# Optimization experiments

Hardware: AMD Instinct MI355X
Metric: run time of the kernel (lower is better)

The kernel has to match this reference:

```python
import jax, jax.numpy as jnp
import numpy as np

B, C, L, H, K, NCONV = 16, 128, 1024, 8, 7, 4
DK = C // H
EPS = 1e-5
NEG = -1e30


def setup_inputs() -> dict:
    key = jax.random.key(0)
    ks = jax.random.split(key, 20)
    s = 0.05
    rn = lambda k, shape: jax.random.normal(k, shape, jnp.float32) * s
    return {
        "x": jax.random.normal(ks[0], (B, C, L), jnp.float32),
        "mask": jax.random.bernoulli(ks[1], 0.1, (B, L)),
        "dw_w": rn(ks[2], (NCONV, C, K)),
        "pw_w": rn(ks[3], (NCONV, C, C)),
        "pw_b": rn(ks[4], (NCONV, C)),
        "ng": jnp.ones((NCONV + 2, C), jnp.float32),
        "nb": jnp.zeros((NCONV + 2, C), jnp.float32),
        "wq": rn(ks[5], (C, C)), "bq": rn(ks[6], (C,)),
        "wk": rn(ks[7], (C, C)), "bk": rn(ks[8], (C,)),
        "wv": rn(ks[9], (C, C)), "bv": rn(ks[10], (C,)),
        "wo": rn(ks[11], (C, C)), "bo": rn(ks[12], (C,)),
        "w1": rn(ks[13], (C, C)), "b1": rn(ks[14], (C,)),
        "w2": rn(ks[15], (C, C)), "b2": rn(ks[16], (C,)),
    }


def _pos_encoding(c, length):
    i = jnp.arange(c, dtype=jnp.float32)
    even = (jnp.arange(c) % 2) == 0
    freq = jnp.where(even, jnp.power(10000.0, -i / c), -jnp.power(10000.0, (1.0 - i) / c))
    phase = jnp.where(even, 0.0, jnp.pi / 2)
    pos = jnp.arange(length, dtype=jnp.float32)
    return jnp.sin(pos[None, :] * freq[:, None] + phase[:, None])  # [C, L]


def _ln(x, g, b):
    # layer norm over channel dim of [B, C, L]
    mu = jnp.mean(x, axis=1, keepdims=True)
    var = jnp.mean(jnp.square(x - mu), axis=1, keepdims=True)
    xn = (x - mu) * jax.lax.rsqrt(var + EPS)
    return xn * g[None, :, None] + b[None, :, None]


def _dsconv(x, dw, pw, pb):
    # depthwise conv1d (groups=C, pad k//2, no bias) + pointwise conv1d (bias)
    y = jax.lax.conv_general_dilated(
        x, dw[:, None, :], window_strides=(1,), padding=[(K // 2, K // 2)],
        feature_group_count=C, dimension_numbers=("NCH", "OIH", "NCH"))
    return jnp.einsum("oc,bcl->bol", pw, y) + pb[None, :, None]


def _attention(x, mask, wq, bq, wk, bk, wv, bv, wo, bo):
    # x: [B, C, L] -> [B, L, C]
    xt = jnp.swapaxes(x, 1, 2)
    q = (xt @ wq.T + bq).reshape(B, L, H, DK)
    k = (xt @ wk.T + bk).reshape(B, L, H, DK)
    v = (xt @ wv.T + bv).reshape(B, L, H, DK)
    scale = 1.0 / np.sqrt(DK)
    scores = jnp.einsum("blhd,bmhd->bhlm", q, k) * scale  # [B, H, L, L]
    scores = jnp.where(mask[:, None, None, :], NEG, scores)
    attn = jax.nn.softmax(scores, axis=-1)
    out = jnp.einsum("bhlm,bmhd->blhd", attn, v).reshape(B, L, C)
    out = out @ wo.T + bo
    return jnp.swapaxes(out, 1, 2)  # [B, C, L]


def reference(x, mask, dw_w, pw_w, pw_b, ng, nb, wq, bq, wk, bk, wv, bv, wo, bo, w1, b1, w2, b2):
    # eval mode: all dropout / stochastic depth are identity
    out = x + _pos_encoding(C, L)[None]
    for i in range(NCONV):
        res = out
        out = _ln(out, ng[i], nb[i])
        out = _dsconv(out, dw_w[i], pw_w[i], pw_b[i])
        out = jax.nn.relu(out)
        out = out + res
    res = out
    out = _ln(out, ng[NCONV], nb[NCONV])
    out = _attention(out, mask, wq, bq, wk, bk, wv, bv, wo, bo)
    out = out + res
    res = out
    out = _ln(out, ng[NCONV + 1], nb[NCONV + 1])
    ot = jnp.swapaxes(out, 1, 2)
    ot = jax.nn.relu(ot @ w1.T + b1)
    ot = ot @ w2.T + b2
    out = jnp.swapaxes(ot, 1, 2) + res
    return out
```

## Files before the change

### kernel.cpp

```cpp
#include <hip/hip_runtime.h>
#include <math.h>


#define ACT_N   2097152
#define OFF_ACT0 0
#define OFF_ACT1 (ACT_N)
#define OFF_QB   (2*ACT_N)
#define OFF_KB   (3*ACT_N)
#define OFF_VT   (4*ACT_N)
#define OFF_ABF  (5*ACT_N)
#define OFF_MF   (6*ACT_N)
#define OFF_WB   (6*ACT_N + 16384)
#define OFF_DW8  (6*ACT_N + 16384 + 81920)

typedef __attribute__((ext_vector_type(8)))  short bf16x8;
typedef __attribute__((ext_vector_type(16))) float f32x16;
typedef __attribute__((ext_vector_type(4)))  float f32x4;

static __device__ __forceinline__ unsigned int f2bf(float f) {
    unsigned int u = __float_as_uint(f);
    return (u + 0x7fffu + ((u >> 16) & 1u)) >> 16;
}
static __device__ __forceinline__ unsigned int pk2(float a, float b) {
    return f2bf(a) | (f2bf(b) << 16);
}

#define GOFF(row, g) (((row) << 8) + ((((g) ^ ((row) & 15))) << 4))

__global__ __launch_bounds__(256) void k_prep(
    const float* __restrict__ pw, const float* __restrict__ wq,
    const float* __restrict__ wk, const float* __restrict__ wv_,
    const float* __restrict__ wo, const float* __restrict__ w1,
    const float* __restrict__ w2, const unsigned char* __restrict__ mask,
    const float* __restrict__ dwsrc,
    unsigned short* __restrict__ wb, float* __restrict__ maskf,
    float* __restrict__ dw8)
{
    int blk = blockIdx.x, t = threadIdx.x;
    if (blk < 10) {
        const float* src;
        if (blk < 4)       src = pw + blk * 16384;
        else if (blk == 4) src = wq;
        else if (blk == 5) src = wk;
        else if (blk == 6) src = wv_;
        else if (blk == 7) src = wo;
        else if (blk == 8) src = w1;
        else               src = w2;
        unsigned short* dst = wb + blk * 16384;
        for (int i = t * 8; i < 16384; i += 2048) {
            float4 a = *(const float4*)(src + i);
            float4 c = *(const float4*)(src + i + 4);
            uint4 v;
            v.x = pk2(a.x, a.y); v.y = pk2(a.z, a.w);
            v.z = pk2(c.x, c.y); v.w = pk2(c.z, c.w);
            *(uint4*)(dst + i) = v;
        }
    } else if (blk == 10) {
        for (int i = t; i < 16384; i += 256)
            maskf[i] = mask[i] ? 0.0f : 1.0f;
    } else {
        for (int i = t; i < 4096; i += 256) {
            int n = i >> 3, tap = i & 7;
            dw8[i] = (tap < 7) ? dwsrc[n * 7 + tap] : 0.0f;
        }
    }
}

__global__ __launch_bounds__(256) void k_pe(const float* __restrict__ x,
                                            float* __restrict__ out)
{
    int idx = blockIdx.x * 256 + threadIdx.x;
    int l = idx & 1023;
    int c = (idx >> 10) & 127;
    float e = (float)(c & ~1);
    float base = exp2f(e * (-13.287712379549449f / 128.0f));
    float freq = (c & 1) ? -base : base;
    float ph   = (c & 1) ? 1.5707963267948966f : 0.0f;
    out[idx] = x[idx] + sinf((float)l * freq + ph);
}

__global__ __launch_bounds__(512) void k_conv(
    const float* __restrict__ in, float* __restrict__ out,
    const unsigned short* __restrict__ wb,
    const float* __restrict__ dw8,
    const float* __restrict__ pb,
    const float* __restrict__ g, const float* __restrict__ nbv)
{
    __shared__ unsigned short Wl[16384];
    __shared__ unsigned short Xl[8192];
    __shared__ float part[560];
    __shared__ float muL[70], rsL[70];

    const int b  = blockIdx.x >> 4;
    const int l0 = (blockIdx.x & 15) << 6;
    const int t  = threadIdx.x;
    const int lane = t & 63;
    const int w = __builtin_amdgcn_readfirstlane(t >> 6);
    const float* xb = in + b * 131072;

    {
        const uint4* src = (const uint4*)wb;
        #pragma unroll
        for (int i = 0; i < 4; ++i) {
            int gi = t + i * 512;
            uint4 v = src[gi];
            int row = gi >> 4, c16 = gi & 15;
            *(uint4*)((char*)Wl + GOFF(row, c16)) = v;
        }
    }
    if (t < 280) {
        int col = t >> 2, sl = t & 3;
        int gl = l0 - 3 + col;
        float s = 0.f, ss = 0.f;
        if ((unsigned)gl < 1024u) {
            for (int c = sl * 32; c < sl * 32 + 32; ++c) {
                float v = xb[c * 1024 + gl];
                s += v; ss = fmaf(v, v, ss);
            }
        }
        part[col * 8 + sl * 2]     = s;
        part[col * 8 + sl * 2 + 1] = ss;
    }
    __syncthreads();
    if (t < 70) {
        int gl = l0 - 3 + t;
        if ((unsigned)gl < 1024u) {
            float s  = part[t*8] + part[t*8+2] + part[t*8+4] + part[t*8+6];
            float ss = part[t*8+1] + part[t*8+3] + part[t*8+5] + part[t*8+7];
            float mu = s * 0.0078125f;
            float var = ss * 0.0078125f - mu * mu;
            muL[t] = mu; rsL[t] = rsqrtf(var + 1e-5f);
        } else { muL[t] = 0.f; rsL[t] = 0.f; }
    }
    __syncthreads();

    {
        const int l = lane;
        const int gl = l0 + l;
        float m[7], rf[7], vm[7];
        int pofs[7];
        #pragma unroll
        for (int j = 0; j < 7; ++j) {
            int p = gl - 3 + j;
            m[j]  = muL[l + j];
            rf[j] = rsL[l + j];
            vm[j] = ((unsigned)p < 1024u) ? 1.f : 0.f;
            pofs[j] = min(max(p, 0), 1023);
        }
        #pragma unroll
        for (int s = 0; s < 2; ++s) {
            int c0 = w * 16 + s * 8;
            unsigned int pk[4];
            #pragma unroll
            for (int cp = 0; cp < 4; ++cp) {
                float y2[2];
                #pragma unroll
                for (int ci = 0; ci < 2; ++ci) {
                    int c = c0 + cp * 2 + ci;
                    const float* xr = xb + c * 1024;
                    const float* dr = dw8 + c * 8;
                    float S1 = 0.f, S2 = 0.f;
                    #pragma unroll
                    for (int j = 0; j < 7; ++j) {
                        float xv = xr[pofs[j]];
                        float u = (xv - m[j]) * rf[j];
                        float dwv = dr[j];
                        S1 = fmaf(dwv, u,     S1);
                        S2 = fmaf(dwv, vm[j], S2);
                    }
                    y2[ci] = g[c] * S1 + nbv[c] * S2;
                }
                pk[cp] = pk2(y2[0], y2[1]);
            }
            *(uint4*)((char*)Xl + GOFF(l, (c0 >> 3))) = *(uint4*)pk;
        }
    }
    __syncthreads();

    const int l31 = lane & 31, hi = lane >> 5;
    const int ow = w >> 1, lh = w & 1;
    bf16x8 af[8];
    #pragma unroll
    for (int kc = 0; kc < 8; ++kc)
        af[kc] = *(const bf16x8*)((char*)Wl + GOFF(ow * 32 + l31, kc * 2 + hi));
    f32x16 acc;
    #pragma unroll
    for (int i = 0; i < 16; ++i) acc[i] = 0.f;
    #pragma unroll
    for (int kc = 0; kc < 8; ++kc) {
        bf16x8 bx = *(const bf16x8*)((char*)Xl + GOFF(lh * 32 + l31, kc * 2 + hi));
        acc = __builtin_amdgcn_mfma_f32_32x32x16_bf16(af[kc], bx, acc, 0, 0, 0);
    }
    float* ob = out + b * 131072;
    const int lg = l0 + lh * 32 + l31;
    #pragma unroll
    for (int r = 0; r < 16; ++r) {
        int o = ow * 32 + (r & 3) + 8 * (r >> 2) + 4 * hi;
        ob[o * 1024 + lg] = fmaxf(acc[r] + pb[o], 0.f) + xb[o * 1024 + lg];
    }
}

__global__ __launch_bounds__(512) void k_qkv(
    const float* __restrict__ in, const unsigned short* __restrict__ wb,
    const float* __restrict__ bq, const float* __restrict__ bk,
    const float* __restrict__ bv,
    const float* __restrict__ g, const float* __restrict__ nbv,
    unsigned short* __restrict__ qb, unsigned short* __restrict__ kb,
    unsigned short* __restrict__ vt)
{
    __shared__ unsigned short Wl[16384];
    __shared__ unsigned short Xl[8192];
    __shared__ unsigned short vs[8][1280];
    __shared__ float part[1024];
    __shared__ float muL[64], rsL[64];

    const int b  = blockIdx.x >> 4;
    const int l0 = (blockIdx.x & 15) << 6;
    const int t  = threadIdx.x;
    const int lane = t & 63;
    const int w = __builtin_amdgcn_readfirstlane(t >> 6);
    const float* xb = in + b * 131072;

    {
        const uint4* src = (const uint4*)wb;
        #pragma unroll
        for (int i = 0; i < 4; ++i) {
            int gi = t + i * 512;
            uint4 v = src[gi];
            int row = gi >> 4, c16 = gi & 15;
            *(uint4*)((char*)Wl + GOFF(row, c16)) = v;
        }
    }
    {
        int col = t >> 3, sl = t & 7;
        float s = 0.f, ss = 0.f;
        for (int c = sl * 16; c < sl * 16 + 16; ++c) {
            float v = xb[c * 1024 + l0 + col];
            s += v; ss = fmaf(v, v, ss);
        }
        part[col * 16 + sl * 2]     = s;
        part[col * 16 + sl * 2 + 1] = ss;
    }
    __syncthreads();
    if (t < 64) {
        float s = 0.f, ss = 0.f;
        #pragma unroll
        for (int j = 0; j < 8; ++j) { s += part[t*16 + j*2]; ss += part[t*16 + j*2 + 1]; }
        float mu = s * 0.0078125f;
        float var = ss * 0.0078125f - mu * mu;
        muL[t] = mu; rsL[t] = rsqrtf(var + 1e-5f);
    }
    __syncthreads();
    {
        const int l = lane;
        float mu = muL[l], rs = rsL[l];
        #pragma unroll
        for (int s = 0; s < 2; ++s) {
            int c0 = w * 16 + s * 8;
            unsigned int pk[4];
            #pragma unroll
            for (int cp = 0; cp < 4; ++cp) {
                int c = c0 + cp * 2;
                float v0 = (xb[c * 1024 + l0 + l]       - mu) * rs * g[c]     + nbv[c];
                float v1 = (xb[(c + 1) * 1024 + l0 + l] - mu) * rs * g[c + 1] + nbv[c + 1];
                pk[cp] = pk2(v0, v1);
            }
            *(uint4*)((char*)Xl + GOFF(l, (c0 >> 3))) = *(uint4*)pk;
        }
    }
    __syncthreads();

    const int l31 = lane & 31, hi = lane >> 5;
    const int ow = w >> 1, lh = w & 1;
    const int lg = l0 + lh * 32 + l31;

    for (int p = 0; p < 3; ++p) {
        uint4 pw4[4];
        if (p < 2) {
            const uint4* src = (const uint4*)(wb + (p + 1) * 16384);
            #pragma unroll
            for (int i = 0; i < 4; ++i) pw4[i] = src[t + i * 512];
        }
        bf16x8 af[8];
        #pragma unroll
        for (int kc = 0; kc < 8; ++kc)
            af[kc] = *(const bf16x8*)((char*)Wl + GOFF(ow * 32 + l31, kc * 2 + hi));
        f32x16 acc;
        #pragma unroll
        for (int i = 0; i < 16; ++i) acc[i] = 0.f;
        #pragma unroll
        for (int kc = 0; kc < 8; ++kc) {
            bf16x8 bx = *(const bf16x8*)((char*)Xl + GOFF(lh * 32 + l31, kc * 2 + hi));
            acc = __builtin_amdgcn_mfma_f32_32x32x16_bf16(af[kc], bx, acc, 0, 0, 0);
        }

        if (p < 2) {
            const float* bias = (p == 0) ? bq : bk;
            unsigned short* dst = (p == 0) ? qb : kb;
            const float scl = (p == 0) ? 0.25f : 1.0f;
            unsigned int pk0[4], pk1[4];
            #pragma unroll
            for (int j2 = 0; j2 < 4; ++j2) {
                int r = j2 * 2;
                int o0 = ow * 32 + (r & 3) + 8 * (r >> 2) + 4 * hi;
                pk0[j2] = pk2((acc[r] + bias[o0]) * scl,
                              (acc[r + 1] + bias[o0 + 1]) * scl);
                int r8 = r + 8;
                int o1 = ow * 32 + (r8 & 3) + 8 * (r8 >> 2) + 4 * hi;
                pk1[j2] = pk2((acc[r8] + bias[o1]) * scl,
                              (acc[r8 + 1] + bias[o1 + 1]) * scl);
            }
            int bh0 = b * 8 + 2 * ow;
            *(uint4*)(dst + ((size_t)bh0 * 1024 + lg) * 16 + hi * 8) = *(uint4*)pk0;
            *(uint4*)(dst + ((size_t)(bh0 + 1) * 1024 + lg) * 16 + hi * 8) = *(uint4*)pk1;
        } else {
            unsigned short* vsw = vs[w];
            #pragma unroll
            for (int r = 0; r < 16; ++r) {
                int orow = (r & 3) + 8 * (r >> 2) + 4 * hi;
                int o = ow * 32 + orow;
                vsw[orow * 40 + l31] = (unsigned short)f2bf(acc[r] + bv[o]);
            }
            int d32 = l31;
            uint4 v0 = *(uint4*)(vsw + d32 * 40 + hi * 16);
            uint4 v1 = *(uint4*)(vsw + d32 * 40 + hi * 16 + 8);
            int head = 2 * ow + (d32 >> 4), dd = d32 & 15;
            unsigned short* vp = vt + ((size_t)(b * 8 + head) * 16 + dd) * 1024
                                    + l0 + lh * 32 + hi * 16;
            *(uint4*)vp = v0; *(uint4*)(vp + 8) = v1;
        }
        __syncthreads();
        if (p < 2) {
            #pragma unroll
            for (int i = 0; i < 4; ++i) {
                int gi = t + i * 512;
                int row = gi >> 4, c16 = gi & 15;
                *(uint4*)((char*)Wl + GOFF(row, c16)) = pw4[i];
            }
            __syncthreads();
        }
    }
}

__global__ __launch_bounds__(256) void k_attn(
    const unsigned short* __restrict__ qb, const unsigned short* __restrict__ kb,
    const unsigned short* __restrict__ vt, const float* __restrict__ mmul,
    unsigned short* __restrict__ abf)
{
    __shared__ unsigned int Kl[8192];
    __shared__ unsigned int Vl[8256];
    __shared__ float        Ml[1024];
    __shared__ unsigned int Pl[4][640];

    const int bh = blockIdx.x >> 3;
    const int b  = bh >> 3;
    const int h  = bh & 7;
    const int qbase = (blockIdx.x & 7) << 7;
    const int t = threadIdx.x;
    const int lane = t & 63;
    const int w = t >> 6;

    {
        const uint4* ksrc = (const uint4*)(kb + (size_t)bh * 16384);
        uint4* kdst = (uint4*)Kl;
        #pragma unroll
        for (int i = 0; i < 8; ++i) kdst[t + i * 256] = ksrc[t + i * 256];
        const unsigned short* vsrc = vt + (size_t)bh * 16384;
        #pragma unroll
        for (int i = 0; i < 8; ++i) {
            int idx = t + i * 256;
            int d = idx >> 7, c = idx & 127;
            uint4 val = *(const uint4*)(vsrc + d * 1024 + c * 8);
            *(uint4*)((char*)Vl + d * 2064 + c * 16) = val;
        }
        ((float4*)Ml)[t] = ((const float4*)(mmul + b * 1024))[t];
    }
    __syncthreads();

    const int l31 = lane & 31, hi = lane >> 5;
    const int l15 = lane & 15, h2 = lane >> 4;
    const int qw = qbase + w * 32;

    bf16x8 qf;
    {
        uint4 qv = *(const uint4*)(qb + ((size_t)bh * 1024 + qw + l31) * 16 + hi * 8);
        union { uint4 u; bf16x8 v; } cvt; cvt.u = qv; qf = cvt.v;
    }

    f32x16 Z;
    #pragma unroll
    for (int i = 0; i < 16; ++i) Z[i] = 0.f;
    f32x4 O0, O1;
    #pragma unroll
    for (int i = 0; i < 4; ++i) { O0[i] = 0.f; O1[i] = 0.f; }
    float sum = 0.f;

    unsigned int* myP = &Pl[w][0];

    for (int kc = 0; kc < 32; ++kc) {
        bf16x8 kf = *(const bf16x8*)((const char*)Kl + (kc * 32 + l31) * 32 + hi * 16);
        f32x16 S = __builtin_amdgcn_mfma_f32_32x32x16_bf16(kf, qf, Z, 0, 0, 0);

        #pragma unroll
        for (int rg = 0; rg < 4; ++rg) {
            float4 mm = *(const float4*)(Ml + kc * 32 + rg * 8 + hi * 4);
            float p0 = __expf(S[rg * 4 + 0]) * mm.x;
            float p1 = __expf(S[rg * 4 + 1]) * mm.y;
            float p2 = __expf(S[rg * 4 + 2]) * mm.z;
            float p3 = __expf(S[rg * 4 + 3]) * mm.w;
            sum += (p0 + p1) + (p2 + p3);
            uint2 pwd;
            pwd.x = (__float_as_uint(p1) & 0xffff0000u) | (__float_as_uint(p0) >> 16);
            pwd.y = (__float_as_uint(p3) & 0xffff0000u) | (__float_as_uint(p2) >> 16);
            *(uint2*)((char*)myP + l31 * 80 + rg * 16 + hi * 8) = pwd;
        }

        bf16x8 vf  = *(const bf16x8*)((const char*)Vl + l15 * 2064 + kc * 64 + h2 * 16);
        bf16x8 pa0 = *(const bf16x8*)((const char*)myP + l15 * 80 + h2 * 16);
        bf16x8 pa1 = *(const bf16x8*)((const char*)myP + (16 + l15) * 80 + h2 * 16);
        O0 = __builtin_amdgcn_mfma_f32_16x16x32_bf16(pa0, vf, O0, 0, 0, 0);
        O1 = __builtin_amdgcn_mfma_f32_16x16x32_bf16(pa1, vf, O1, 0, 0, 0);
    }

    sum += __shfl_xor(sum, 32);
    float inv = 1.0f / sum;

    #pragma unroll
    for (int r = 0; r < 4; ++r) {
        float iv0 = __shfl(inv, h2 * 4 + r);
        float iv1 = __shfl(inv, 16 + h2 * 4 + r);
        myP[(h2 * 4 + r) * 17 + l15]      = __float_as_uint(O0[r] * iv0);
        myP[(16 + h2 * 4 + r) * 17 + l15] = __float_as_uint(O1[r] * iv1);
    }
    unsigned int pk4[4];
    #pragma unroll
    for (int j2 = 0; j2 < 4; ++j2) {
        float a0 = __uint_as_float(myP[l31 * 17 + hi * 8 + j2 * 2]);
        float a1 = __uint_as_float(myP[l31 * 17 + hi * 8 + j2 * 2 + 1]);
        pk4[j2] = pk2(a0, a1);
    }
    unsigned short* op = abf + ((size_t)(b * 1024 + qw + l31)) * 128 + h * 16 + hi * 8;
    *(uint4*)op = *(uint4*)pk4;
}

__global__ __launch_bounds__(512) void k_oproj(
    const unsigned short* __restrict__ abf, const unsigned short* __restrict__ wb,
    const float* __restrict__ bo, const float* __restrict__ res,
    float* __restrict__ out)
{
    __shared__ unsigned short Wl[16384];
    __shared__ unsigned short Xl[8192];
    const int b  = blockIdx.x >> 4;
    const int l0 = (blockIdx.x & 15) << 6;
    const int t  = threadIdx.x;
    const int lane = t & 63;
    const int w = __builtin_amdgcn_readfirstlane(t >> 6);

    {
        const uint4* src = (const uint4*)wb;
        #pragma unroll
        for (int i = 0; i < 4; ++i) {
            int gi = t + i * 512;
            uint4 v = src[gi];
            int row = gi >> 4, c16 = gi & 15;
            *(uint4*)((char*)Wl + GOFF(row, c16)) = v;
        }
        #pragma unroll
        for (int i = 0; i < 2; ++i) {
            int gi = t + i * 512;
            int row = gi >> 4, c16 = gi & 15;
            uint4 v = *(const uint4*)(abf + ((size_t)(b * 1024 + l0 + row)) * 128 + c16 * 8);
            *(uint4*)((char*)Xl + GOFF(row, c16)) = v;
        }
    }
    __syncthreads();

    const int l31 = lane & 31, hi = lane >> 5;
    const int ow = w >> 1, lh = w & 1;
    bf16x8 af[8];
    #pragma unroll
    for (int kc = 0; kc < 8; ++kc)
        af[kc] = *(const bf16x8*)((char*)Wl + GOFF(ow * 32 + l31, kc * 2 + hi));
    f32x16 acc;
    #pragma unroll
    for (int i = 0; i < 16; ++i) acc[i] = 0.f;
    #pragma unroll
    for (int kc = 0; kc < 8; ++kc) {
        bf16x8 bx = *(const bf16x8*)((char*)Xl + GOFF(lh * 32 + l31, kc * 2 + hi));
        acc = __builtin_amdgcn_mfma_f32_32x32x16_bf16(af[kc], bx, acc, 0, 0, 0);
    }
    const float* rb = res + b * 131072;
    float* ob = out + b * 131072;
    const int lg = l0 + lh * 32 + l31;
    #pragma unroll
    for (int r = 0; r < 16; ++r) {
        int o = ow * 32 + (r & 3) + 8 * (r >> 2) + 4 * hi;
        ob[o * 1024 + lg] = acc[r] + bo[o] + rb[o * 1024 + lg];
    }
}

__global__ __launch_bounds__(512) void k_ffn(
    const float* __restrict__ in,
    const unsigned short* __restrict__ w1b, const unsigned short* __restrict__ w2b,
    const float* __restrict__ b1, const float* __restrict__ b2,
    const float* __restrict__ g, const float* __restrict__ nbv,
    float* __restrict__ out)
{
    __shared__ unsigned short Wl[16384];
    __shared__ unsigned short Xl[8192];
    __shared__ unsigned short Xl2[8192];
    __shared__ float part[1024];
    __shared__ float muL[64], rsL[64];

    const int b  = blockIdx.x >> 4;
    const int l0 = (blockIdx.x & 15) << 6;
    const int t  = threadIdx.x;
    const int lane = t & 63;
    const int w = __builtin_amdgcn_readfirstlane(t >> 6);
    const float* xb = in + b * 131072;

    {
        const uint4* src = (const uint4*)w1b;
        #pragma unroll
        for (int i = 0; i < 4; ++i) {
            int gi = t + i * 512;
            uint4 v = src[gi];
            int row = gi >> 4, c16 = gi & 15;
            *(uint4*)((char*)Wl + GOFF(row, c16)) = v;
        }
    }
    {
        int col = t >> 3, sl = t & 7;
        float s = 0.f, ss = 0.f;
        for (int c = sl * 16; c < sl * 16 + 16; ++c) {
            float v = xb[c * 1024 + l0 + col];
            s += v; ss = fmaf(v, v, ss);
        }
        part[col * 16 + sl * 2]     = s;
        part[col * 16 + sl * 2 + 1] = ss;
    }
    __syncthreads();
    if (t < 64) {
        float s = 0.f, ss = 0.f;
        #pragma unroll
        for (int j = 0; j < 8; ++j) { s += part[t*16 + j*2]; ss += part[t*16 + j*2 + 1]; }
        float mu = s * 0.0078125f;
        float var = ss * 0.0078125f - mu * mu;
        muL[t] = mu; rsL[t] = rsqrtf(var + 1e-5f);
    }
    __syncthreads();
    {
        const int l = lane;
        float mu = muL[l], rs = rsL[l];
        #pragma unroll
        for (int s = 0; s < 2; ++s) {
            int c0 = w * 16 + s * 8;
            unsigned int pk[4];
            #pragma unroll
            for (int cp = 0; cp < 4; ++cp) {
                int c = c0 + cp * 2;
                float v0 = (xb[c * 1024 + l0 + l]       - mu) * rs * g[c]     + nbv[c];
                float v1 = (xb[(c + 1) * 1024 + l0 + l] - mu) * rs * g[c + 1] + nbv[c + 1];
                pk[cp] = pk2(v0, v1);
            }
            *(uint4*)((char*)Xl + GOFF(l, (c0 >> 3))) = *(uint4*)pk;
        }
    }
    __syncthreads();

    const int l31 = lane & 31, hi = lane >> 5;
    const int ow = w >> 1, lh = w & 1;
    const int lrow = lh * 32 + l31;

    uint4 pw4[4];
    {
        const uint4* src = (const uint4*)w2b;
        #pragma unroll
        for (int i = 0; i < 4; ++i) pw4[i] = src[t + i * 512];
    }
    {
        bf16x8 af[8];
        #pragma unroll
        for (int kc = 0; kc < 8; ++kc)
            af[kc] = *(const bf16x8*)((char*)Wl + GOFF(ow * 32 + l31, kc * 2 + hi));
        f32x16 acc;
        #pragma unroll
        for (int i = 0; i < 16; ++i) acc[i] = 0.f;
        #pragma unroll
        for (int kc = 0; kc < 8; ++kc) {
            bf16x8 bx = *(const bf16x8*)((char*)Xl + GOFF(lrow, kc * 2 + hi));
            acc = __builtin_amdgcn_mfma_f32_32x32x16_bf16(af[kc], bx, acc, 0, 0, 0);
        }
        #pragma unroll
        for (int r = 0; r < 16; ++r) {
            int o = ow * 32 + (r & 3) + 8 * (r >> 2) + 4 * hi;
            float hval = fmaxf(acc[r] + b1[o], 0.f);
            *(unsigned short*)((char*)Xl2 + (lrow << 8)
                + ((((o >> 3) ^ (lrow & 15))) << 4) + ((o & 7) * 2)) =
                (unsigned short)f2bf(hval);
        }
    }
    __syncthreads();
    {
        #pragma unroll
        for (int i = 0; i < 4; ++i) {
            int gi = t + i * 512;
            int row = gi >> 4, c16 = gi & 15;
            *(uint4*)((char*)Wl + GOFF(row, c16)) = pw4[i];
        }
    }
    __syncthreads();
    {
        bf16x8 af[8];
        #pragma unroll
        for (int kc = 0; kc < 8; ++kc)
            af[kc] = *(const bf16x8*)((char*)Wl + GOFF(ow * 32 + l31, kc * 2 + hi));
        f32x16 acc;
        #pragma unroll
        for (int i = 0; i < 16; ++i) acc[i] = 0.f;
        #pragma unroll
        for (int kc = 0; kc < 8; ++kc) {
            bf16x8 bx = *(const bf16x8*)((char*)Xl2 + GOFF(lrow, kc * 2 + hi));
            acc = __builtin_amdgcn_mfma_f32_32x32x16_bf16(af[kc], bx, acc, 0, 0, 0);
        }
        float* ob = out + b * 131072;
        const int lg = l0 + lrow;
        #pragma unroll
        for (int r = 0; r < 16; ++r) {
            int o = ow * 32 + (r & 3) + 8 * (r >> 2) + 4 * hi;
            ob[o * 1024 + lg] = acc[r] + b2[o] + xb[o * 1024 + lg];
        }
    }
}

extern "C" void kernel_launch(void* const* d_in, const int* in_sizes, int n_in,
                              void* d_out, int out_size, void* d_ws, size_t ws_size,
                              hipStream_t stream)
{
    const float* x    = (const float*)d_in[0];
    const unsigned char* mask = (const unsigned char*)d_in[1];
    const float* dw_w = (const float*)d_in[2];
    const float* pw_w = (const float*)d_in[3];
    const float* pw_b = (const float*)d_in[4];
    const float* ng   = (const float*)d_in[5];
    const float* nb   = (const float*)d_in[6];
    const float* wq   = (const float*)d_in[7];
    const float* bq   = (const float*)d_in[8];
    const float* wk   = (const float*)d_in[9];
    const float* bk   = (const float*)d_in[10];
    const float* wv   = (const float*)d_in[11];
    const float* bv   = (const float*)d_in[12];
    const float* wo   = (const float*)d_in[13];
    const float* bo   = (const float*)d_in[14];
    const float* w1   = (const float*)d_in[15];
    const float* b1   = (const float*)d_in[16];
    const float* w2   = (const float*)d_in[17];
    const float* b2   = (const float*)d_in[18];

    float* ws   = (float*)d_ws;
    float* act0 = ws + OFF_ACT0;
    float* act1 = ws + OFF_ACT1;
    unsigned short* qb  = (unsigned short*)(ws + OFF_QB);
    unsigned short* kbp = (unsigned short*)(ws + OFF_KB);
    unsigned short* vtp = (unsigned short*)(ws + OFF_VT);
    unsigned short* abf = (unsigned short*)(ws + OFF_ABF);
    float* mf   = ws + OFF_MF;
    unsigned short* wb = (unsigned short*)(ws + OFF_WB);
    float* dw8  = ws + OFF_DW8;

    k_prep<<<12, 256, 0, stream>>>(pw_w, wq, wk, wv, wo, w1, w2, mask, dw_w,
                                   wb, mf, dw8);
    k_pe<<<8192, 256, 0, stream>>>(x, act0);

    k_conv<<<256, 512, 0, stream>>>(act0, act1, wb + 0 * 16384, dw8 + 0,
                                    pw_b + 0,   ng + 0,   nb + 0);
    k_conv<<<256, 512, 0, stream>>>(act1, act0, wb + 1 * 16384, dw8 + 1024,
                                    pw_b + 128, ng + 128, nb + 128);
    k_conv<<<256, 512, 0, stream>>>(act0, act1, wb + 2 * 16384, dw8 + 2048,
                                    pw_b + 256, ng + 256, nb + 256);
    k_conv<<<256, 512, 0, stream>>>(act1, act0, wb + 3 * 16384, dw8 + 3072,
                                    pw_b + 384, ng + 384, nb + 384);

    k_qkv<<<256, 512, 0, stream>>>(act0, wb + 4 * 16384, bq, bk, bv,
                                   ng + 4 * 128, nb + 4 * 128, qb, kbp, vtp);
    k_attn<<<1024, 256, 0, stream>>>(qb, kbp, vtp, mf, abf);
    k_oproj<<<256, 512, 0, stream>>>(abf, wb + 7 * 16384, bo, act0, act1);
    k_ffn<<<256, 512, 0, stream>>>(act1, wb + 8 * 16384, wb + 9 * 16384,
                                   b1, b2, ng + 5 * 128, nb + 5 * 128,
                                   (float*)d_out);
}
```

Before: 224.3 us.

## Double-buffer K/V in attention, fold scale into exp2, vectorize PE kernel

The attention kernel now streams K and V in four double-buffered chunks, issuing the global loads for the next chunk before computing the current one instead of loading the whole head into LDS up front. The log2(e) factor is folded into the Q scale so it can use exp2f, and the mask becomes an additive -inf-like bias. Row sums are computed with extra MFMAs against a ones vector rather than scalar adds plus a shuffle. Normalization uses a fast reciprocal and packs bf16 through a smaller LDS tile. Separately, the positional-encoding kernel is vectorized to float4 with a quarter of the blocks. These changes add register pressure and extra MFMA work, and the sum is now taken over bf16-rounded probabilities, which slightly changes numerics.

```diff
diff --git a/kernel.cpp b/kernel.cpp
--- a/kernel.cpp
+++ b/kernel.cpp
@@ -26,6 +26,8 @@
 }
 
 #define GOFF(row, g) (((row) << 8) + ((((g) ^ ((row) & 15))) << 4))
+
+#define QSCALE 0.3606737602222409f
 
 __global__ __launch_bounds__(256) void k_prep(
     const float* __restrict__ pw, const float* __restrict__ wq,
@@ -57,7 +59,7 @@
         }
     } else if (blk == 10) {
         for (int i = t; i < 16384; i += 256)
-            maskf[i] = mask[i] ? 0.0f : 1.0f;
+            maskf[i] = mask[i] ? -3.0e38f : 0.0f;
     } else {
         for (int i = t; i < 4096; i += 256) {
             int n = i >> 3, tap = i & 7;
@@ -69,14 +71,21 @@
 __global__ __launch_bounds__(256) void k_pe(const float* __restrict__ x,
                                             float* __restrict__ out)
 {
-    int idx = blockIdx.x * 256 + threadIdx.x;
-    int l = idx & 1023;
-    int c = (idx >> 10) & 127;
+    int i4 = blockIdx.x * 256 + threadIdx.x;
+    int base = i4 * 4;
+    int l = base & 1023;
+    int c = (base >> 10) & 127;
     float e = (float)(c & ~1);
-    float base = exp2f(e * (-13.287712379549449f / 128.0f));
-    float freq = (c & 1) ? -base : base;
+    float fb = exp2f(e * (-13.287712379549449f / 128.0f));
+    float freq = (c & 1) ? -fb : fb;
     float ph   = (c & 1) ? 1.5707963267948966f : 0.0f;
-    out[idx] = x[idx] + sinf((float)l * freq + ph);
+    float4 xv = ((const float4*)x)[i4];
+    float4 o;
+    o.x = xv.x + sinf((float)l * freq + ph);
+    o.y = xv.y + sinf((float)(l + 1) * freq + ph);
+    o.z = xv.z + sinf((float)(l + 2) * freq + ph);
+    o.w = xv.w + sinf((float)(l + 3) * freq + ph);
+    ((float4*)out)[i4] = o;
 }
 
 __global__ __launch_bounds__(512) void k_conv(
@@ -297,7 +306,7 @@
         if (p < 2) {
             const float* bias = (p == 0) ? bq : bk;
             unsigned short* dst = (p == 0) ? qb : kb;
-            const float scl = (p == 0) ? 0.25f : 1.0f;
+            const float scl = (p == 0) ? QSCALE : 1.0f;
             unsigned int pk0[4], pk1[4];
             #pragma unroll
             for (int j2 = 0; j2 < 4; ++j2) {
@@ -344,12 +353,12 @@
 
 __global__ __launch_bounds__(256) void k_attn(
     const unsigned short* __restrict__ qb, const unsigned short* __restrict__ kb,
-    const unsigned short* __restrict__ vt, const float* __restrict__ mmul,
+    const unsigned short* __restrict__ vt, const float* __restrict__ madd,
     unsigned short* __restrict__ abf)
 {
-    __shared__ unsigned int Kl[8192];
-    __shared__ unsigned int Vl[8256];
-    __shared__ float        Ml[1024];
+    __shared__ unsigned short Kl[2][4096];
+    __shared__ unsigned short Vl[2][4224];
+    __shared__ float Ml[1024];
     __shared__ unsigned int Pl[4][640];
 
     const int bh = blockIdx.x >> 3;
@@ -359,88 +368,115 @@
     const int t = threadIdx.x;
     const int lane = t & 63;
     const int w = t >> 6;
-
-    {
-        const uint4* ksrc = (const uint4*)(kb + (size_t)bh * 16384);
-        uint4* kdst = (uint4*)Kl;
-        #pragma unroll
-        for (int i = 0; i < 8; ++i) kdst[t + i * 256] = ksrc[t + i * 256];
-        const unsigned short* vsrc = vt + (size_t)bh * 16384;
-        #pragma unroll
-        for (int i = 0; i < 8; ++i) {
-            int idx = t + i * 256;
-            int d = idx >> 7, c = idx & 127;
-            uint4 val = *(const uint4*)(vsrc + d * 1024 + c * 8);
-            *(uint4*)((char*)Vl + d * 2064 + c * 16) = val;
-        }
-        ((float4*)Ml)[t] = ((const float4*)(mmul + b * 1024))[t];
-    }
-    __syncthreads();
-
     const int l31 = lane & 31, hi = lane >> 5;
     const int l15 = lane & 15, h2 = lane >> 4;
     const int qw = qbase + w * 32;
 
+    const uint4* ksrc = (const uint4*)(kb + (size_t)bh * 16384);
+    const unsigned short* vsrc = vt + (size_t)bh * 16384;
+
+    const int d0v = t >> 5,          ko0 = t & 31;
+    const int d1v = (t + 256) >> 5,  ko1 = (t + 256) & 31;
+    const int kp0 = t & 1,        kk0 = t >> 1;
+    const int kp1 = t & 1,        kk1 = (t + 256) >> 1;
+
+    ((float4*)Ml)[t] = ((const float4*)(madd + b * 1024))[t];
+
     bf16x8 qf;
     {
         uint4 qv = *(const uint4*)(qb + ((size_t)bh * 1024 + qw + l31) * 16 + hi * 8);
         union { uint4 u; bf16x8 v; } cvt; cvt.u = qv; qf = cvt.v;
     }
+    bf16x8 ones;
+    #pragma unroll
+    for (int i = 0; i < 8; ++i) ones[i] = (short)0x3F80;
+
+    {
+        uint4 kr0 = ksrc[t], kr1 = ksrc[t + 256];
+        uint4 vr0 = *(const uint4*)(vsrc + d0v * 1024 + ko0 * 8);
+        uint4 vr1 = *(const uint4*)(vsrc + d1v * 1024 + ko1 * 8);
+        *(uint4*)(&Kl[0][kp0 * 2048 + kk0 * 8]) = kr0;
+        *(uint4*)(&Kl[0][kp1 * 2048 + kk1 * 8]) = kr1;
+        *(uint4*)(&Vl[0][d0v * 264 + ko0 * 8]) = vr0;
+        *(uint4*)(&Vl[0][d1v * 264 + ko1 * 8]) = vr1;
+    }
+    __syncthreads();
 
     f32x16 Z;
     #pragma unroll
     for (int i = 0; i < 16; ++i) Z[i] = 0.f;
-    f32x4 O0, O1;
-    #pragma unroll
-    for (int i = 0; i < 4; ++i) { O0[i] = 0.f; O1[i] = 0.f; }
-    float sum = 0.f;
+    f32x4 O0, O1, Os0, Os1;
+    #pragma unroll
+    for (int i = 0; i < 4; ++i) { O0[i] = 0.f; O1[i] = 0.f; Os0[i] = 0.f; Os1[i] = 0.f; }
 
     unsigned int* myP = &Pl[w][0];
-
-    for (int kc = 0; kc < 32; ++kc) {
-        bf16x8 kf = *(const bf16x8*)((const char*)Kl + (kc * 32 + l31) * 32 + hi * 16);
-        f32x16 S = __builtin_amdgcn_mfma_f32_32x32x16_bf16(kf, qf, Z, 0, 0, 0);
-
-        #pragma unroll
-        for (int rg = 0; rg < 4; ++rg) {
-            float4 mm = *(const float4*)(Ml + kc * 32 + rg * 8 + hi * 4);
-            float p0 = __expf(S[rg * 4 + 0]) * mm.x;
-            float p1 = __expf(S[rg * 4 + 1]) * mm.y;
-            float p2 = __expf(S[rg * 4 + 2]) * mm.z;
-            float p3 = __expf(S[rg * 4 + 3]) * mm.w;
-            sum += (p0 + p1) + (p2 + p3);
-            uint2 pwd;
-            pwd.x = (__float_as_uint(p1) & 0xffff0000u) | (__float_as_uint(p0) >> 16);
-            pwd.y = (__float_as_uint(p3) & 0xffff0000u) | (__float_as_uint(p2) >> 16);
-            *(uint2*)((char*)myP + l31 * 80 + rg * 16 + hi * 8) = pwd;
-        }
-
-        bf16x8 vf  = *(const bf16x8*)((const char*)Vl + l15 * 2064 + kc * 64 + h2 * 16);
-        bf16x8 pa0 = *(const bf16x8*)((const char*)myP + l15 * 80 + h2 * 16);
-        bf16x8 pa1 = *(const bf16x8*)((const char*)myP + (16 + l15) * 80 + h2 * 16);
-        O0 = __builtin_amdgcn_mfma_f32_16x16x32_bf16(pa0, vf, O0, 0, 0, 0);
-        O1 = __builtin_amdgcn_mfma_f32_16x16x32_bf16(pa1, vf, O1, 0, 0, 0);
-    }
-
-    sum += __shfl_xor(sum, 32);
-    float inv = 1.0f / sum;
-
+    int cur = 0;
+
+    for (int ch = 0; ch < 4; ++ch) {
+        uint4 kr0, kr1, vr0, vr1;
+        if (ch < 3) {
+            int cb = (ch + 1) * 512;
+            int vb = (ch + 1) * 256;
+            kr0 = ksrc[cb + t];
+            kr1 = ksrc[cb + t + 256];
+            vr0 = *(const uint4*)(vsrc + d0v * 1024 + vb + ko0 * 8);
+            vr1 = *(const uint4*)(vsrc + d1v * 1024 + vb + ko1 * 8);
+        }
+        const unsigned short* Kb = Kl[cur];
+        const unsigned short* Vb = Vl[cur];
+        const int kgbase = ch * 256;
+
+        #pragma unroll 2
+        for (int kc = 0; kc < 8; ++kc) {
+            bf16x8 kf = *(const bf16x8*)(Kb + hi * 2048 + (kc * 32 + l31) * 8);
+            f32x16 S = __builtin_amdgcn_mfma_f32_32x32x16_bf16(kf, qf, Z, 0, 0, 0);
+
+            #pragma unroll
+            for (int rg = 0; rg < 4; ++rg) {
+                float4 mm = *(const float4*)(Ml + kgbase + kc * 32 + rg * 8 + hi * 4);
+                float p0 = exp2f(S[rg * 4 + 0] + mm.x);
+                float p1 = exp2f(S[rg * 4 + 1] + mm.y);
+                float p2 = exp2f(S[rg * 4 + 2] + mm.z);
+                float p3 = exp2f(S[rg * 4 + 3] + mm.w);
+                uint2 pwd;
+                pwd.x = __builtin_amdgcn_perm(__float_as_uint(p1),
+                                              __float_as_uint(p0), 0x07060302u);
+                pwd.y = __builtin_amdgcn_perm(__float_as_uint(p3),
+                                              __float_as_uint(p2), 0x07060302u);
+                *(uint2*)((char*)myP + l31 * 80 + rg * 16 + hi * 8) = pwd;
+            }
+
+            bf16x8 vf  = *(const bf16x8*)(Vb + l15 * 264 + kc * 32 + h2 * 8);
+            bf16x8 pa0 = *(const bf16x8*)((const char*)myP + l15 * 80 + h2 * 16);
+            bf16x8 pa1 = *(const bf16x8*)((const char*)myP + (16 + l15) * 80 + h2 * 16);
+            O0  = __builtin_amdgcn_mfma_f32_16x16x32_bf16(pa0, vf,   O0,  0, 0, 0);
+            O1  = __builtin_amdgcn_mfma_f32_16x16x32_bf16(pa1, vf,   O1,  0, 0, 0);
+            Os0 = __builtin_amdgcn_mfma_f32_16x16x32_bf16(pa0, ones, Os0, 0, 0, 0);
+            Os1 = __builtin_amdgcn_mfma_f32_16x16x32_bf16(pa1, ones, Os1, 0, 0, 0);
+        }
+
+        if (ch < 3) {
+            __syncthreads();
+            int nxt = cur ^ 1;
+            *(uint4*)(&Kl[nxt][kp0 * 2048 + kk0 * 8]) = kr0;
+            *(uint4*)(&Kl[nxt][kp1 * 2048 + kk1 * 8]) = kr1;
+            *(uint4*)(&Vl[nxt][d0v * 264 + ko0 * 8]) = vr0;
+            *(uint4*)(&Vl[nxt][d1v * 264 + ko1 * 8]) = vr1;
+            __syncthreads();
+            cur = nxt;
+        }
+    }
+
+    unsigned short* myP16 = (unsigned short*)myP;
     #pragma unroll
     for (int r = 0; r < 4; ++r) {
-        float iv0 = __shfl(inv, h2 * 4 + r);
-        float iv1 = __shfl(inv, 16 + h2 * 4 + r);
-        myP[(h2 * 4 + r) * 17 + l15]      = __float_as_uint(O0[r] * iv0);
-        myP[(16 + h2 * 4 + r) * 17 + l15] = __float_as_uint(O1[r] * iv1);
-    }
-    unsigned int pk4[4];
-    #pragma unroll
-    for (int j2 = 0; j2 < 4; ++j2) {
-        float a0 = __uint_as_float(myP[l31 * 17 + hi * 8 + j2 * 2]);
-        float a1 = __uint_as_float(myP[l31 * 17 + hi * 8 + j2 * 2 + 1]);
-        pk4[j2] = pk2(a0, a1);
-    }
-    unsigned short* op = abf + ((size_t)(b * 1024 + qw + l31)) * 128 + h * 16 + hi * 8;
-    *(uint4*)op = *(uint4*)pk4;
+        float i0 = __builtin_amdgcn_rcpf(Os0[r] + 1e-37f);
+        float i1 = __builtin_amdgcn_rcpf(Os1[r] + 1e-37f);
+        myP16[(h2 * 4 + r) * 20 + l15]        = (unsigned short)f2bf(O0[r] * i0);
+        myP16[(16 + h2 * 4 + r) * 20 + l15]   = (unsigned short)f2bf(O1[r] * i1);
+    }
+    uint4 ov = *(const uint4*)(myP16 + l31 * 20 + hi * 8);
+    *(uint4*)(abf + ((size_t)(b * 1024 + qw + l31)) * 128 + h * 16 + hi * 8) = ov;
 }
 
 __global__ __launch_bounds__(512) void k_oproj(
@@ -670,7 +706,7 @@
 
     k_prep<<<12, 256, 0, stream>>>(pw_w, wq, wk, wv, wo, w1, w2, mask, dw_w,
                                    wb, mf, dw8);
-    k_pe<<<8192, 256, 0, stream>>>(x, act0);
+    k_pe<<<2048, 256, 0, stream>>>(x, act0);
 
     k_conv<<<256, 512, 0, stream>>>(act0, act1, wb + 0 * 16384, dw8 + 0,
                                     pw_b + 0,   ng + 0,   nb + 0);
```

Measured after the change: 225.7 us. About the same (+0.6%).
